# Performance work log

Hardware: AMD Instinct MI355X
Metric: run time of the kernel (lower is better)

The kernel has to match this reference:

```python
import jax, jax.numpy as jnp
import numpy as np

N = 400000      # active voxels
C_IN = 64
C_OUT = 64
GRID = 128      # voxel grid extent per axis
K = 3           # kernel size -> 27 offsets
EPS = 1e-5      # BatchNorm eps


def _build_neighbor_map():
    """Kernel map for stride-1 sparse conv: nmap[k, i] = input voxel index at
    coords[i] + offset[k], or -1 if that voxel is inactive / out of bounds."""
    rng = np.random.default_rng(0)
    raw = rng.integers(0, GRID, size=(3 * N // 2, 3))
    keys = (raw[:, 0] * GRID + raw[:, 1]) * GRID + raw[:, 2]
    ukeys = np.unique(keys)
    assert len(ukeys) >= N
    ukeys = ukeys[:N]  # sorted voxel keys of the N active sites
    x = ukeys // (GRID * GRID)
    y = (ukeys // GRID) % GRID
    z = ukeys % GRID
    r = np.arange(-(K // 2), K // 2 + 1)
    offs = np.stack(np.meshgrid(r, r, r, indexing="ij"), -1).reshape(-1, 3)
    nmap = np.full((offs.shape[0], N), -1, dtype=np.int32)
    for k, (dx, dy, dz) in enumerate(offs):
        nx, ny, nz = x + dx, y + dy, z + dz
        inb = (nx >= 0) & (nx < GRID) & (ny >= 0) & (ny < GRID) & (nz >= 0) & (nz < GRID)
        qk = (nx * GRID + ny) * GRID + nz
        pos = np.clip(np.searchsorted(ukeys, qk), 0, N - 1)
        hit = inb & (ukeys[pos] == qk)
        nmap[k] = np.where(hit, pos, -1).astype(np.int32)
    return jnp.asarray(nmap)


def setup_inputs() -> dict:
    key = jax.random.key(0)
    k1, k2 = jax.random.split(key)
    features = jax.random.normal(k1, (N, C_IN), jnp.float32)
    neighbor_map = _build_neighbor_map()  # [27, N] int32
    fan_in = C_IN * K ** 3
    weight = jax.random.normal(k2, (K ** 3, C_IN, C_OUT), jnp.float32) * (1.0 / np.sqrt(fan_in))
    gamma = jnp.ones((C_OUT,), jnp.float32)
    beta = jnp.zeros((C_OUT,), jnp.float32)
    return {"features": features, "neighbor_map": neighbor_map,
            "weight": weight, "gamma": gamma, "beta": beta}


def _sparse_conv(features, neighbor_map, weight):
    # gather-GEMM-scatter, accumulated over the 27 kernel offsets via scan
    n = features.shape[0]
    def step(acc, inp):
        idx, w_k = inp                                    # [N], [C_in, C_out]
        safe = jnp.maximum(idx, 0)
        g = jnp.where((idx >= 0)[:, None], features[safe], 0.0)  # gather [N, C_in]
        return acc + g @ w_k, None
    init = jnp.zeros((n, weight.shape[-1]), features.dtype)
    out, _ = jax.lax.scan(step, init, (neighbor_map, weight))
    return out


def reference(features, neighbor_map, weight, gamma, beta):
    out = _sparse_conv(features, neighbor_map, weight)   # [N, C_out]
    mean = out.mean(axis=0)                              # BatchNorm (training stats)
    var = out.var(axis=0)
    y = (out - mean) * jax.lax.rsqrt(var + EPS) * gamma + beta
    return jnp.maximum(y, 0.0)                           # ReLU
```

## Files before the change

### kernel.cpp

```cpp
#include <hip/hip_runtime.h>

#define NVOX 400000
#define K27 27
#define EPS_ 1e-5f

typedef short short8 __attribute__((ext_vector_type(8)));
typedef float floatx4 __attribute__((ext_vector_type(4)));
typedef unsigned int uintx4 __attribute__((ext_vector_type(4)));

__device__ __forceinline__ unsigned int pack2bf(float a, float b) {
    unsigned int ua = __builtin_bit_cast(unsigned int, a);
    unsigned int ub = __builtin_bit_cast(unsigned int, b);
    ua += 0x7fffu + ((ua >> 16) & 1u);
    ub += 0x7fffu + ((ub >> 16) & 1u);
    return (ua >> 16) | (ub & 0xffff0000u);
}

__device__ __forceinline__ void gload_lds16(const void* g, void* l) {
    __builtin_amdgcn_global_load_lds(
        (const __attribute__((address_space(1))) void*)g,
        (__attribute__((address_space(3))) void*)l, 16, 0, 0);
}

__global__ void prep_kernel(const float* __restrict__ w,
                            const float* __restrict__ feat,
                            unsigned short* __restrict__ feat_bf,
                            unsigned short* __restrict__ wt,
                            float* __restrict__ sums,
                            float* __restrict__ zrow,
                            int fb) {
    const int b = blockIdx.x;
    const int t = threadIdx.x;
    if (b < fb) {
#pragma unroll
        for (int r = 0; r < 4; ++r) {
            const int i0 = b * 8192 + r * 2048 + t * 8;
            const floatx4* s = (const floatx4*)(feat + i0);
            const floatx4 f0 = s[0], f1 = s[1];
            uintx4 v;
            v[0] = pack2bf(f0[0], f0[1]); v[1] = pack2bf(f0[2], f0[3]);
            v[2] = pack2bf(f1[0], f1[1]); v[3] = pack2bf(f1[2], f1[3]);
            *(uintx4*)(feat_bf + i0) = v;
        }
    } else if (b < fb + 32) {
        for (int g = (b - fb) * 256 + t; g < K27 * 64 * 64; g += 32 * 256) {
            const int k = g >> 12, r = g & 4095, co = r >> 6, ci = r & 63;
            unsigned int u =
                __builtin_bit_cast(unsigned int, w[(k << 12) + (ci << 6) + co]);
            u += 0x7fffu + ((u >> 16) & 1u);
            wt[g] = (unsigned short)(u >> 16);
        }
    } else {
        if (t < 128) sums[t] = 0.0f;
        else if (zrow && t < 136) zrow[t - 128] = 0.0f;
    }
}

template <bool BF16FEAT>
__launch_bounds__(256)
__global__ void conv_mfma(const float* __restrict__ feat,
                          const unsigned short* __restrict__ feat_bf,
                          const int* __restrict__ nmap,
                          const unsigned short* __restrict__ wt,
                          const unsigned short* __restrict__ zrow,
                          float* __restrict__ out,
                          float* __restrict__ sums) {
    __shared__ __align__(16) unsigned short a_tile[2][128 * 64];
    __shared__ __align__(16) unsigned short b_tile[2][64 * 64];
    __shared__ float cstat[128];

    const int tid  = threadIdx.x;
    const int wv   = tid >> 6;
    const int lane = tid & 63;
    const int m    = lane & 15;
    const int q    = lane >> 4;

    const int nwg = gridDim.x;
    const int q8 = nwg >> 3, r8 = nwg & 7;
    const int xcd = blockIdx.x & 7, lin = blockIdx.x >> 3;
    const int wg =
        (xcd < r8 ? xcd * (q8 + 1) : r8 * (q8 + 1) + (xcd - r8) * q8) + lin;
    const int base = wg * 128;

    if (tid < 128) cstat[tid] = 0.0f;

    int row_a[2];
#pragma unroll
    for (int mt = 0; mt < 2; ++mt) row_a[mt] = wv * 32 + mt * 16 + m;

    floatx4 acc[2][4];
#pragma unroll
    for (int mt = 0; mt < 2; ++mt)
#pragma unroll
        for (int nt = 0; nt < 4; ++nt)
            acc[mt][nt] = (floatx4){0.f, 0.f, 0.f, 0.f};

#define STAGE_G(bufidx, kk)                                                   \
    do {                                                                      \
        _Pragma("unroll") for (int j = 0; j < 4; ++j) {                       \
            const int blk = j * 4 + wv;                                       \
            const int row = blk * 8 + (lane >> 3);                            \
            const int gc  = (lane & 7) ^ (row & 7);                           \
            const int ix  = nmap[(size_t)(kk) * NVOX + base + row];           \
            const unsigned short* src =                                       \
                (ix >= 0) ? feat_bf + (size_t)ix * 64 + gc * 8 : zrow;        \
            gload_lds16(src, a_tile[bufidx] + blk * 512);                     \
        }                                                                     \
        _Pragma("unroll") for (int j = 0; j < 2; ++j) {                       \
            const int blk = j * 4 + wv;                                       \
            const int row = blk * 8 + (lane >> 3);                            \
            const int gc  = (lane & 7) ^ (row & 7);                           \
            gload_lds16(wt + (kk)*4096 + row * 64 + gc * 8,                   \
                        b_tile[bufidx] + blk * 512);                          \
        }                                                                     \
    } while (0)

#define COMPUTE(bufidx)                                                       \
    do {                                                                      \
        _Pragma("unroll") for (int kb = 0; kb < 2; ++kb) {                    \
            short8 af[2], bf[4];                                              \
            _Pragma("unroll") for (int mt = 0; mt < 2; ++mt)                  \
                af[mt] = *(const short8*)(                                    \
                    a_tile[bufidx] +                                          \
                    (row_a[mt] * 8 + ((kb * 4 + q) ^ (row_a[mt] & 7))) * 8);  \
            _Pragma("unroll") for (int nt = 0; nt < 4; ++nt) {                \
                const int row = nt * 16 + m;                                  \
                bf[nt] = *(const short8*)(                                    \
                    b_tile[bufidx] +                                          \
                    (row * 8 + ((kb * 4 + q) ^ (row & 7))) * 8);              \
            }                                                                 \
            _Pragma("unroll") for (int mt = 0; mt < 2; ++mt)                  \
                _Pragma("unroll") for (int nt = 0; nt < 4; ++nt)              \
                    acc[mt][nt] = __builtin_amdgcn_mfma_f32_16x16x32_bf16(    \
                        af[mt], bf[nt], acc[mt][nt], 0, 0, 0);                \
        }                                                                     \
    } while (0)

    if constexpr (BF16FEAT) {
        __syncthreads();
        STAGE_G(0, 0);
        __syncthreads();
        for (int kk = 0; kk < K27; kk += 2) {
            if (kk + 1 < K27) STAGE_G(1, kk + 1);
            COMPUTE(0);
            __syncthreads();
            if (kk + 1 >= K27) break;
            if (kk + 2 < K27) STAGE_G(0, kk + 2);
            COMPUTE(1);
            __syncthreads();
        }
    } else {
        for (int kk = 0; kk < K27; ++kk) {
            short8 areg[4], breg[2];
            int arow[4];
#pragma unroll
            for (int j = 0; j < 4; ++j) {
                const int c = tid + 256 * j;
                arow[j] = c >> 3;
                const int gcs = c & 7;
                const int ix = nmap[(size_t)kk * NVOX + base + arow[j]];
                areg[j] = (short8){0, 0, 0, 0, 0, 0, 0, 0};
                if (ix >= 0) {
                    const float* fp = feat + (size_t)ix * 64 + gcs * 8;
                    const floatx4 f0 = *(const floatx4*)fp;
                    const floatx4 f1 = *(const floatx4*)(fp + 4);
                    uintx4 v;
                    v[0] = pack2bf(f0[0], f0[1]); v[1] = pack2bf(f0[2], f0[3]);
                    v[2] = pack2bf(f1[0], f1[1]); v[3] = pack2bf(f1[2], f1[3]);
                    areg[j] = __builtin_bit_cast(short8, v);
                }
            }
#pragma unroll
            for (int j = 0; j < 2; ++j) {
                const int c = tid + 256 * j;
                breg[j] = *(const short8*)(wt + kk * 4096 + c * 8);
            }
            __syncthreads();
#pragma unroll
            for (int j = 0; j < 4; ++j) {
                const int c = tid + 256 * j;
                *(short8*)(a_tile[0] +
                           (arow[j] * 8 + ((c & 7) ^ (arow[j] & 7))) * 8) =
                    areg[j];
            }
#pragma unroll
            for (int j = 0; j < 2; ++j) {
                const int c = tid + 256 * j;
                const int br = c >> 3;
                *(short8*)(b_tile[0] + (br * 8 + ((c & 7) ^ (br & 7))) * 8) =
                    breg[j];
            }
            __syncthreads();
            COMPUTE(0);
        }
    }
#undef STAGE_G
#undef COMPUTE

#pragma unroll
    for (int nt = 0; nt < 4; ++nt) {
        const int col = nt * 16 + m;
        float s = 0.f, s2 = 0.f;
#pragma unroll
        for (int mt = 0; mt < 2; ++mt) {
            const int row0 = base + wv * 32 + mt * 16 + q * 4;
#pragma unroll
            for (int i = 0; i < 4; ++i) {
                const float v = acc[mt][nt][i];
                s += v;
                s2 += v * v;
                out[(size_t)(row0 + i) * 64 + col] = v;
            }
        }
        atomicAdd(&cstat[col], s);
        atomicAdd(&cstat[64 + col], s2);
    }
    __syncthreads();
    if (tid < 128) atomicAdd(&sums[tid], cstat[tid]);
}

__global__ void bn_apply(float* __restrict__ out, const float* __restrict__ sums,
                         const float* __restrict__ gamma,
                         const float* __restrict__ beta) {
    __shared__ float sc[64];
    __shared__ float sh[64];
    const int tid = threadIdx.x;
    if (tid < 64) {
        const float inv_n = 1.0f / (float)NVOX;
        const float mean = sums[tid] * inv_n;
        const float var  = sums[64 + tid] * inv_n - mean * mean;
        const float g    = gamma[tid] * rsqrtf(var + EPS_);
        sc[tid] = g;
        sh[tid] = beta[tid] - mean * g;
    }
    __syncthreads();
    const int cg = (tid & 15) * 4;
    floatx4 scale, shift;
#pragma unroll
    for (int j = 0; j < 4; ++j) {
        scale[j] = sc[cg + j];
        shift[j] = sh[cg + j];
    }
    floatx4* p = (floatx4*)out;
    const int total4 = NVOX * 16;
    for (int i = blockIdx.x * 256 + tid; i < total4; i += gridDim.x * 256) {
        floatx4 v = p[i] * scale + shift;
#pragma unroll
        for (int j = 0; j < 4; ++j) v[j] = v[j] > 0.f ? v[j] : 0.f;
        p[i] = v;
    }
}

extern "C" void kernel_launch(void* const* d_in, const int* in_sizes, int n_in,
                              void* d_out, int out_size, void* d_ws, size_t ws_size,
                              hipStream_t stream) {
    const float* feat  = (const float*)d_in[0];
    const int*   nmap  = (const int*)d_in[1];
    const float* w     = (const float*)d_in[2];
    const float* gamma = (const float*)d_in[3];
    const float* beta  = (const float*)d_in[4];
    float* out = (float*)d_out;

    const size_t FEATB = (size_t)NVOX * 64 * 2;
    const size_t WTB   = (size_t)K27 * 64 * 64 * 2;
    const int conv_blocks = NVOX / 128;

    if (ws_size >= FEATB + WTB + 512 + 128) {
        unsigned short* feat_bf = (unsigned short*)d_ws;
        unsigned short* wt      = (unsigned short*)((char*)d_ws + FEATB);
        float* sums             = (float*)((char*)d_ws + FEATB + WTB);
        float* zrow             = (float*)((char*)d_ws + FEATB + WTB + 512);
        prep_kernel<<<dim3(3158), dim3(256), 0, stream>>>(
            w, feat, feat_bf, wt, sums, zrow, 3125);
        conv_mfma<true><<<dim3(conv_blocks), dim3(256), 0, stream>>>(
            feat, feat_bf, nmap, wt, (const unsigned short*)zrow, out, sums);
        bn_apply<<<dim3(1024), dim3(256), 0, stream>>>(out, sums, gamma, beta);
    } else {
        unsigned short* wt = (unsigned short*)d_ws;
        float* sums        = (float*)((char*)d_ws + WTB);
        prep_kernel<<<dim3(33), dim3(256), 0, stream>>>(
            w, feat, nullptr, wt, sums, nullptr, 0);
        conv_mfma<false><<<dim3(conv_blocks), dim3(256), 0, stream>>>(
            feat, nullptr, nmap, wt, nullptr, out, sums);
        bn_apply<<<dim3(1024), dim3(256), 0, stream>>>(out, sums, gamma, beta);
    }
}
```

Before: 444.0 us.

## Halve conv tile to 64 rows, read weights from global, prefetch neighbor indices to LDS

```diff
diff --git a/kernel.cpp b/kernel.cpp
--- a/kernel.cpp
+++ b/kernel.cpp
@@ -57,7 +57,7 @@
 }
 
 template <bool BF16FEAT>
-__launch_bounds__(256)
+__launch_bounds__(128)
 __global__ void conv_mfma(const float* __restrict__ feat,
                           const unsigned short* __restrict__ feat_bf,
                           const int* __restrict__ nmap,
@@ -65,8 +65,8 @@
                           const unsigned short* __restrict__ zrow,
                           float* __restrict__ out,
                           float* __restrict__ sums) {
-    __shared__ __align__(16) unsigned short a_tile[2][128 * 64];
-    __shared__ __align__(16) unsigned short b_tile[2][64 * 64];
+    __shared__ __align__(16) unsigned short a_tile[2][64 * 64];
+    __shared__ int idx_lds[K27 * 64];
     __shared__ float cstat[128];
 
     const int tid  = threadIdx.x;
@@ -80,9 +80,18 @@
     const int xcd = blockIdx.x & 7, lin = blockIdx.x >> 3;
     const int wg =
         (xcd < r8 ? xcd * (q8 + 1) : r8 * (q8 + 1) + (xcd - r8) * q8) + lin;
-    const int base = wg * 128;
-
-    if (tid < 128) cstat[tid] = 0.0f;
+    const int base = wg * 64;
+
+    for (int j = tid; j < K27 * 64; j += 128)
+        idx_lds[j] = nmap[(size_t)(j >> 6) * NVOX + base + (j & 63)];
+    cstat[tid] = 0.0f;
+    __syncthreads();
+
+    const int rsub = lane >> 3;
+    const int gcx  = (lane & 7) ^ rsub;
+    int arow[4];
+#pragma unroll
+    for (int j = 0; j < 4; ++j) arow[j] = j * 16 + wv * 8 + rsub;
 
     int row_a[2];
 #pragma unroll
@@ -95,72 +104,62 @@
         for (int nt = 0; nt < 4; ++nt)
             acc[mt][nt] = (floatx4){0.f, 0.f, 0.f, 0.f};
 
-#define STAGE_G(bufidx, kk)                                                   \
+#define STAGE_A(bufidx, kk)                                                   \
     do {                                                                      \
+        int ixr[4];                                                           \
+        _Pragma("unroll") for (int j = 0; j < 4; ++j)                         \
+            ixr[j] = idx_lds[(kk) * 64 + arow[j]];                            \
         _Pragma("unroll") for (int j = 0; j < 4; ++j) {                       \
-            const int blk = j * 4 + wv;                                       \
-            const int row = blk * 8 + (lane >> 3);                            \
-            const int gc  = (lane & 7) ^ (row & 7);                           \
-            const int ix  = nmap[(size_t)(kk) * NVOX + base + row];           \
             const unsigned short* src =                                       \
-                (ix >= 0) ? feat_bf + (size_t)ix * 64 + gc * 8 : zrow;        \
-            gload_lds16(src, a_tile[bufidx] + blk * 512);                     \
-        }                                                                     \
-        _Pragma("unroll") for (int j = 0; j < 2; ++j) {                       \
-            const int blk = j * 4 + wv;                                       \
-            const int row = blk * 8 + (lane >> 3);                            \
-            const int gc  = (lane & 7) ^ (row & 7);                           \
-            gload_lds16(wt + (kk)*4096 + row * 64 + gc * 8,                   \
-                        b_tile[bufidx] + blk * 512);                          \
+                (ixr[j] >= 0) ? feat_bf + (size_t)ixr[j] * 64 + gcx * 8       \
+                              : zrow;                                         \
+            gload_lds16(src, a_tile[bufidx] + (j * 128 + wv * 64) * 8);       \
         }                                                                     \
     } while (0)
 
-#define COMPUTE(bufidx)                                                       \
+#define COMPUTE(bufidx, kk)                                                   \
     do {                                                                      \
+        const unsigned short* bp = wt + (size_t)(kk) * 4096 + m * 64 + q * 8; \
         _Pragma("unroll") for (int kb = 0; kb < 2; ++kb) {                    \
-            short8 af[2], bf[4];                                              \
+            short8 af[2], bfr[4];                                             \
             _Pragma("unroll") for (int mt = 0; mt < 2; ++mt)                  \
                 af[mt] = *(const short8*)(                                    \
                     a_tile[bufidx] +                                          \
                     (row_a[mt] * 8 + ((kb * 4 + q) ^ (row_a[mt] & 7))) * 8);  \
-            _Pragma("unroll") for (int nt = 0; nt < 4; ++nt) {                \
-                const int row = nt * 16 + m;                                  \
-                bf[nt] = *(const short8*)(                                    \
-                    b_tile[bufidx] +                                          \
-                    (row * 8 + ((kb * 4 + q) ^ (row & 7))) * 8);              \
-            }                                                                 \
+            _Pragma("unroll") for (int nt = 0; nt < 4; ++nt)                  \
+                bfr[nt] = *(const short8*)(bp + nt * 1024 + kb * 32);         \
             _Pragma("unroll") for (int mt = 0; mt < 2; ++mt)                  \
                 _Pragma("unroll") for (int nt = 0; nt < 4; ++nt)              \
                     acc[mt][nt] = __builtin_amdgcn_mfma_f32_16x16x32_bf16(    \
-                        af[mt], bf[nt], acc[mt][nt], 0, 0, 0);                \
+                        af[mt], bfr[nt], acc[mt][nt], 0, 0, 0);               \
         }                                                                     \
     } while (0)
 
     if constexpr (BF16FEAT) {
-        __syncthreads();
-        STAGE_G(0, 0);
+        STAGE_A(0, 0);
         __syncthreads();
         for (int kk = 0; kk < K27; kk += 2) {
-            if (kk + 1 < K27) STAGE_G(1, kk + 1);
-            COMPUTE(0);
+            if (kk + 1 < K27) STAGE_A(1, kk + 1);
+            COMPUTE(0, kk);
             __syncthreads();
             if (kk + 1 >= K27) break;
-            if (kk + 2 < K27) STAGE_G(0, kk + 2);
-            COMPUTE(1);
+            if (kk + 2 < K27) STAGE_A(0, kk + 2);
+            COMPUTE(1, kk + 1);
             __syncthreads();
         }
     } else {
         for (int kk = 0; kk < K27; ++kk) {
-            short8 areg[4], breg[2];
-            int arow[4];
+            short8 areg[4];
+            int farow[4], fslot[4];
 #pragma unroll
             for (int j = 0; j < 4; ++j) {
-                const int c = tid + 256 * j;
-                arow[j] = c >> 3;
-                const int gcs = c & 7;
-                const int ix = nmap[(size_t)kk * NVOX + base + arow[j]];
+                const int c = tid + 128 * j;
+                farow[j] = c >> 3;
+                fslot[j] = c & 7;
+                const int ix = idx_lds[kk * 64 + farow[j]];
                 areg[j] = (short8){0, 0, 0, 0, 0, 0, 0, 0};
                 if (ix >= 0) {
+                    const int gcs = fslot[j] ^ (farow[j] & 7);
                     const float* fp = feat + (size_t)ix * 64 + gcs * 8;
                     const floatx4 f0 = *(const floatx4*)fp;
                     const floatx4 f1 = *(const floatx4*)(fp + 4);
@@ -170,31 +169,16 @@
                     areg[j] = __builtin_bit_cast(short8, v);
                 }
             }
-#pragma unroll
-            for (int j = 0; j < 2; ++j) {
-                const int c = tid + 256 * j;
-                breg[j] = *(const short8*)(wt + kk * 4096 + c * 8);
-            }
-            __syncthreads();
-#pragma unroll
-            for (int j = 0; j < 4; ++j) {
-                const int c = tid + 256 * j;
-                *(short8*)(a_tile[0] +
-                           (arow[j] * 8 + ((c & 7) ^ (arow[j] & 7))) * 8) =
+            __syncthreads();
+#pragma unroll
+            for (int j = 0; j < 4; ++j)
+                *(short8*)(a_tile[0] + (farow[j] * 8 + fslot[j]) * 8) =
                     areg[j];
-            }
-#pragma unroll
-            for (int j = 0; j < 2; ++j) {
-                const int c = tid + 256 * j;
-                const int br = c >> 3;
-                *(short8*)(b_tile[0] + (br * 8 + ((c & 7) ^ (br & 7))) * 8) =
-                    breg[j];
-            }
-            __syncthreads();
-            COMPUTE(0);
-        }
-    }
-#undef STAGE_G
+            __syncthreads();
+            COMPUTE(0, kk);
+        }
+    }
+#undef STAGE_A
 #undef COMPUTE
 
 #pragma unroll
@@ -263,7 +247,7 @@
 
     const size_t FEATB = (size_t)NVOX * 64 * 2;
     const size_t WTB   = (size_t)K27 * 64 * 64 * 2;
-    const int conv_blocks = NVOX / 128;
+    const int conv_blocks = NVOX / 64;
 
     if (ws_size >= FEATB + WTB + 512 + 128) {
         unsigned short* feat_bf = (unsigned short*)d_ws;
@@ -272,7 +256,7 @@
         float* zrow             = (float*)((char*)d_ws + FEATB + WTB + 512);
         prep_kernel<<<dim3(3158), dim3(256), 0, stream>>>(
             w, feat, feat_bf, wt, sums, zrow, 3125);
-        conv_mfma<true><<<dim3(conv_blocks), dim3(256), 0, stream>>>(
+        conv_mfma<true><<<dim3(conv_blocks), dim3(128), 0, stream>>>(
             feat, feat_bf, nmap, wt, (const unsigned short*)zrow, out, sums);
         bn_apply<<<dim3(1024), dim3(256), 0, stream>>>(out, sums, gamma, beta);
     } else {
@@ -280,7 +264,7 @@
         float* sums        = (float*)((char*)d_ws + WTB);
         prep_kernel<<<dim3(33), dim3(256), 0, stream>>>(
             w, feat, nullptr, wt, sums, nullptr, 0);
-        conv_mfma<false><<<dim3(conv_blocks), dim3(256), 0, stream>>>(
+        conv_mfma<false><<<dim3(conv_blocks), dim3(128), 0, stream>>>(
             feat, nullptr, nmap, wt, nullptr, out, sums);
         bn_apply<<<dim3(1024), dim3(256), 0, stream>>>(out, sums, gamma, beta);
     }
```

After: 620.1 us. 1.4x slower.

## Prefetch neighbor indices into LDS three offsets ahead of the feature gather

Applied to the files above, without the earlier changes.

```diff
diff --git a/kernel.cpp b/kernel.cpp
--- a/kernel.cpp
+++ b/kernel.cpp
@@ -67,6 +67,7 @@
                           float* __restrict__ sums) {
     __shared__ __align__(16) unsigned short a_tile[2][128 * 64];
     __shared__ __align__(16) unsigned short b_tile[2][64 * 64];
+    __shared__ __align__(16) int idx_w[3 * 128];
     __shared__ float cstat[128];
 
     const int tid  = threadIdx.x;
@@ -84,6 +85,12 @@
 
     if (tid < 128) cstat[tid] = 0.0f;
 
+    const int rsub = lane >> 3;
+    const int gcx  = (lane & 7) ^ rsub;
+    int arow[4];
+#pragma unroll
+    for (int j = 0; j < 4; ++j) arow[j] = (j * 4 + wv) * 8 + rsub;
+
     int row_a[2];
 #pragma unroll
     for (int mt = 0; mt < 2; ++mt) row_a[mt] = wv * 32 + mt * 16 + m;
@@ -95,70 +102,96 @@
         for (int nt = 0; nt < 4; ++nt)
             acc[mt][nt] = (floatx4){0.f, 0.f, 0.f, 0.f};
 
-#define STAGE_G(bufidx, kk)                                                   \
-    do {                                                                      \
-        _Pragma("unroll") for (int j = 0; j < 4; ++j) {                       \
-            const int blk = j * 4 + wv;                                       \
-            const int row = blk * 8 + (lane >> 3);                            \
-            const int gc  = (lane & 7) ^ (row & 7);                           \
-            const int ix  = nmap[(size_t)(kk) * NVOX + base + row];           \
-            const unsigned short* src =                                       \
-                (ix >= 0) ? feat_bf + (size_t)ix * 64 + gc * 8 : zrow;        \
-            gload_lds16(src, a_tile[bufidx] + blk * 512);                     \
-        }                                                                     \
-        _Pragma("unroll") for (int j = 0; j < 2; ++j) {                       \
-            const int blk = j * 4 + wv;                                       \
-            const int row = blk * 8 + (lane >> 3);                            \
-            const int gc  = (lane & 7) ^ (row & 7);                           \
-            gload_lds16(wt + (kk)*4096 + row * 64 + gc * 8,                   \
-                        b_tile[bufidx] + blk * 512);                          \
-        }                                                                     \
-    } while (0)
-
-#define COMPUTE(bufidx)                                                       \
+#define COMPUTE(bufidx, kk)                                                   \
     do {                                                                      \
         _Pragma("unroll") for (int kb = 0; kb < 2; ++kb) {                    \
-            short8 af[2], bf[4];                                              \
+            short8 af[2], bfr[4];                                             \
             _Pragma("unroll") for (int mt = 0; mt < 2; ++mt)                  \
                 af[mt] = *(const short8*)(                                    \
                     a_tile[bufidx] +                                          \
                     (row_a[mt] * 8 + ((kb * 4 + q) ^ (row_a[mt] & 7))) * 8);  \
             _Pragma("unroll") for (int nt = 0; nt < 4; ++nt) {                \
                 const int row = nt * 16 + m;                                  \
-                bf[nt] = *(const short8*)(                                    \
+                bfr[nt] = *(const short8*)(                                   \
                     b_tile[bufidx] +                                          \
                     (row * 8 + ((kb * 4 + q) ^ (row & 7))) * 8);              \
             }                                                                 \
             _Pragma("unroll") for (int mt = 0; mt < 2; ++mt)                  \
                 _Pragma("unroll") for (int nt = 0; nt < 4; ++nt)              \
                     acc[mt][nt] = __builtin_amdgcn_mfma_f32_16x16x32_bf16(    \
-                        af[mt], bf[nt], acc[mt][nt], 0, 0, 0);                \
+                        af[mt], bfr[nt], acc[mt][nt], 0, 0, 0);               \
         }                                                                     \
     } while (0)
 
     if constexpr (BF16FEAT) {
+#define STAGE(bufidx, t, rs)                                                  \
+    do {                                                                      \
+        _Pragma("unroll") for (int j = 0; j < 2; ++j) {                       \
+            const int brw = (j * 4 + wv) * 8 + rsub;                          \
+            gload_lds16(wt + (size_t)(t) * 4096 + brw * 64 + gcx * 8,         \
+                        b_tile[bufidx] + (j * 4 + wv) * 512);                 \
+        }                                                                     \
+        int ixr[4];                                                           \
+        _Pragma("unroll") for (int j = 0; j < 4; ++j)                         \
+            ixr[j] = idx_w[(rs) * 128 + arow[j]];                             \
+        _Pragma("unroll") for (int j = 0; j < 4; ++j) {                       \
+            const unsigned short* src =                                       \
+                (ixr[j] >= 0) ? feat_bf + (size_t)ixr[j] * 64 + gcx * 8       \
+                              : zrow;                                         \
+            gload_lds16(src, a_tile[bufidx] + (j * 4 + wv) * 512);            \
+        }                                                                     \
+    } while (0)
+
+#define GIDX(t)                                                               \
+    do {                                                                      \
+        if (tid < 32)                                                         \
+            gload_lds16(nmap + (size_t)(t) * NVOX + base + tid * 4,           \
+                        idx_w + ((t) % 3) * 128);                             \
+    } while (0)
+
+        GIDX(1);
+        GIDX(2);
+        {
+            int i0[4];
+#pragma unroll
+            for (int j = 0; j < 4; ++j)
+                i0[j] = nmap[(size_t)0 * NVOX + base + arow[j]];
+#pragma unroll
+            for (int j = 0; j < 2; ++j) {
+                const int brw = (j * 4 + wv) * 8 + rsub;
+                gload_lds16(wt + brw * 64 + gcx * 8,
+                            b_tile[0] + (j * 4 + wv) * 512);
+            }
+#pragma unroll
+            for (int j = 0; j < 4; ++j) {
+                const unsigned short* src =
+                    (i0[j] >= 0) ? feat_bf + (size_t)i0[j] * 64 + gcx * 8
+                                 : zrow;
+                gload_lds16(src, a_tile[0] + (j * 4 + wv) * 512);
+            }
+        }
         __syncthreads();
-        STAGE_G(0, 0);
-        __syncthreads();
-        for (int kk = 0; kk < K27; kk += 2) {
-            if (kk + 1 < K27) STAGE_G(1, kk + 1);
-            COMPUTE(0);
+
+#pragma unroll
+        for (int kk = 0; kk < K27; ++kk) {
+            const int bufC = kk & 1;
+            if (kk + 1 < K27) STAGE(bufC ^ 1, kk + 1, (kk + 1) % 3);
+            if (kk + 3 < K27) GIDX(kk + 3);
+            COMPUTE(bufC, kk);
             __syncthreads();
-            if (kk + 1 >= K27) break;
-            if (kk + 2 < K27) STAGE_G(0, kk + 2);
-            COMPUTE(1);
-            __syncthreads();
-        }
+        }
+#undef GIDX
+#undef STAGE
     } else {
         for (int kk = 0; kk < K27; ++kk) {
             short8 areg[4], breg[2];
-            int arow[4];
+            int farow[4];
 #pragma unroll
             for (int j = 0; j < 4; ++j) {
                 const int c = tid + 256 * j;
-                arow[j] = c >> 3;
+                farow[j] = c >> 3;
                 const int gcs = c & 7;
-                const int ix = nmap[(size_t)kk * NVOX + base + arow[j]];
+                const int ix = nmap[(size_t)kk * NVOX + base + farow[j]];
                 areg[j] = (short8){0, 0, 0, 0, 0, 0, 0, 0};
                 if (ix >= 0) {
                     const float* fp = feat + (size_t)ix * 64 + gcs * 8;
@@ -180,7 +213,7 @@
             for (int j = 0; j < 4; ++j) {
                 const int c = tid + 256 * j;
                 *(short8*)(a_tile[0] +
-                           (arow[j] * 8 + ((c & 7) ^ (arow[j] & 7))) * 8) =
+                           (farow[j] * 8 + ((c & 7) ^ (farow[j] & 7))) * 8) =
                     areg[j];
             }
 #pragma unroll
@@ -191,10 +224,9 @@
                     breg[j];
             }
             __syncthreads();
-            COMPUTE(0);
-        }
-    }
-#undef STAGE_G
+            COMPUTE(0, kk);
+        }
+    }
 #undef COMPUTE
 
 #pragma unroll
```

Result: faster. 391.1 us (-11.9%).
